# Optimization experiments

Hardware: AMD Instinct MI355X
Metric: run time of the kernel (lower is better)

Reference implementation:

```python
import jax, jax.numpy as jnp
import numpy as np

C = 1280  # layers_dim[1]


def setup_inputs() -> dict:
    key = jax.random.key(0)
    ks = jax.random.split(key, 8)
    E, N, H, W = 8192, 1024, 4, 4
    pose = jax.random.normal(ks[0], (E, 9), dtype=jnp.float32)
    image = jax.random.normal(ks[1], (N, C, H, W), dtype=jnp.float32)
    # edge_encoder params: Linear(9,1280) -> ReLU -> Linear(1280,2560) -> Sigmoid
    W1 = jax.random.normal(ks[2], (9, C), dtype=jnp.float32) * (1.0 / np.sqrt(9))
    b1 = jnp.zeros((C,), dtype=jnp.float32)
    W2 = jax.random.normal(ks[3], (C, 2 * C), dtype=jnp.float32) * (1.0 / np.sqrt(C))
    b2 = jnp.zeros((2 * C,), dtype=jnp.float32)
    src = jax.random.randint(ks[4], (E,), 0, N)
    dst = jax.random.randint(ks[5], (E,), 0, N)
    return {"pose": pose, "image": image, "W1": W1, "b1": b1,
            "W2": W2, "b2": b2, "src": src, "dst": dst}


def reference(pose, image, W1, b1, W2, b2, src, dst):
    # edge encoder: MLP -> sigmoid -> interleaved (gamma, beta) per channel
    h = jax.nn.relu(pose @ W1 + b1)                        # [E, C]
    e = jax.nn.sigmoid(h @ W2 + b2).reshape(-1, C, 2)      # [E, C, 2]
    gamma = e[:, :, 0][:, :, None, None]                   # [E, C, 1, 1]
    beta = e[:, :, 1][:, :, None, None]                    # [E, C, 1, 1]
    # per-edge message: affine transform of source node feature map
    m = gamma * image[src] + beta                          # [E, C, H, W]
    N = image.shape[0]
    s = jax.ops.segment_sum(m, dst, num_segments=N)        # [N, C, H, W]
    cnt = jax.ops.segment_sum(jnp.ones((m.shape[0],), m.dtype), dst,
                              num_segments=N)              # [N]
    cnt4 = cnt[:, None, None, None]
    # mean over mailbox; nodes with no incoming edges stay zero (DGL default)
    return jnp.where(cnt4 > 0, s / jnp.maximum(cnt4, 1.0), 0.0)
```

## Files before the change

### kernel.cpp

```cpp
#include <hip/hip_runtime.h>

#define C_DIM 1280
#define K_DIM 1280
#define N_DIM 2560
#define HWSZ 16
#define CHW (C_DIM*HWSZ)

#define GBM 256
#define GBN 320
#define GBK 64
#define GNT (K_DIM / GBK)

#define EPB 32
#define NBC 2048

typedef __bf16 bf16;
typedef __attribute__((ext_vector_type(8))) __bf16 bf16x8;
typedef __attribute__((ext_vector_type(4))) __bf16 bf16x4;
typedef __attribute__((ext_vector_type(8))) unsigned short u16x8;
typedef __attribute__((ext_vector_type(4))) float f32x4;

template<int V> struct IC { static constexpr int v = V; };

__device__ __forceinline__ void gload_lds16(const void* g, void* l) {
  __builtin_amdgcn_global_load_lds(
      (const __attribute__((address_space(1))) void*)g,
      (__attribute__((address_space(3))) void*)l, 16, 0, 0);
}

#define SB __builtin_amdgcn_sched_barrier(0)

__global__ __launch_bounds__(256) void prep(
    const float* __restrict__ pose, const float* __restrict__ W1,
    const float* __restrict__ b1, bf16* __restrict__ h,
    const float* __restrict__ W2, bf16* __restrict__ W2t,
    const float* __restrict__ img32, bf16* __restrict__ imgb,
    const int* __restrict__ dst, const int* __restrict__ src,
    int* __restrict__ offsets, int2* __restrict__ pairs, int E, int N)
{
  const int b = blockIdx.x;
  const int t = threadIdx.x;
  const int NBP = (E / EPB) * 5;
  const int NBT = (N_DIM / 32) * (K_DIM / 32);

  if (b == 0) {
    __shared__ int cnt[1024];
    __shared__ int cur[1024];
    __shared__ int wsum[4];
    #pragma unroll
    for (int i = 0; i < 4; ++i) cnt[t + 256 * i] = 0;
    __syncthreads();
    const int4* dst4 = (const int4*)dst;
    const int4* src4 = (const int4*)src;
    const int E4 = E >> 2;
    for (int e4 = t; e4 < E4; e4 += 256) {
      const int4 d = dst4[e4];
      atomicAdd(&cnt[d.x], 1); atomicAdd(&cnt[d.y], 1);
      atomicAdd(&cnt[d.z], 1); atomicAdd(&cnt[d.w], 1);
    }
    __syncthreads();
    const int s0 = cnt[4*t], s1 = cnt[4*t+1], s2 = cnt[4*t+2], s3 = cnt[4*t+3];
    const int tot = s0 + s1 + s2 + s3;
    const int lane = t & 63, w = t >> 6;
    int x = tot;
    #pragma unroll
    for (int off = 1; off < 64; off <<= 1) {
      int y = __shfl_up(x, off);
      if (lane >= off) x += y;
    }
    if (lane == 63) wsum[w] = x;
    __syncthreads();
    int woff = 0;
    for (int i = 0; i < w; ++i) woff += wsum[i];
    const int excl = x + woff - tot;
    const int o0 = excl, o1 = o0 + s0, o2 = o1 + s1, o3 = o2 + s2;
    offsets[4*t] = o0; offsets[4*t+1] = o1; offsets[4*t+2] = o2; offsets[4*t+3] = o3;
    cur[4*t] = o0; cur[4*t+1] = o1; cur[4*t+2] = o2; cur[4*t+3] = o3;
    if (t == 0) offsets[N] = E;
    __syncthreads();
    for (int e4 = t; e4 < E4; e4 += 256) {
      const int4 d = dst4[e4];
      const int4 s = src4[e4];
      const int e = e4 * 4;
      int p;
      p = atomicAdd(&cur[d.x], 1); pairs[p] = make_int2(e,     s.x);
      p = atomicAdd(&cur[d.y], 1); pairs[p] = make_int2(e + 1, s.y);
      p = atomicAdd(&cur[d.z], 1); pairs[p] = make_int2(e + 2, s.z);
      p = atomicAdd(&cur[d.w], 1); pairs[p] = make_int2(e + 3, s.w);
    }
    return;
  }

  const int pb = b - 1;
  if (pb < NBP) {
    const int eg = pb / 5;
    const int cc = pb % 5;
    const int c  = cc * 256 + t;
    const int e0 = eg * EPB;
    float w[9];
    #pragma unroll
    for (int k = 0; k < 9; ++k) w[k] = W1[k * C_DIM + c];
    const float bias = b1[c];
    #pragma unroll 4
    for (int i = 0; i < EPB; ++i) {
      const float* p = pose + (size_t)(e0 + i) * 9;
      float s = bias;
      #pragma unroll
      for (int k = 0; k < 9; ++k) s += p[k] * w[k];
      s = s > 0.f ? s : 0.f;
      h[(size_t)(e0 + i) * C_DIM + c] = (bf16)s;
    }
    return;
  }

  if (pb < NBP + NBT) {
    const int tb = pb - NBP;
    __shared__ float tile[32][33];
    const int n0 = (tb % (N_DIM / 32)) * 32;
    const int k0 = (tb / (N_DIM / 32)) * 32;
    const int r  = t >> 3;
    const int c4 = (t & 7) * 4;
    const f32x4 v = *(const f32x4*)(W2 + (size_t)(k0 + r) * N_DIM + n0 + c4);
    tile[r][c4] = v[0]; tile[r][c4+1] = v[1]; tile[r][c4+2] = v[2]; tile[r][c4+3] = v[3];
    __syncthreads();
    bf16x4 o;
    o[0] = (bf16)tile[c4+0][r];
    o[1] = (bf16)tile[c4+1][r];
    o[2] = (bf16)tile[c4+2][r];
    o[3] = (bf16)tile[c4+3][r];
    *(bf16x4*)(W2t + (size_t)(n0 + r) * K_DIM + k0 + c4) = o;
    return;
  }

  const int cb = pb - NBP - NBT;
  f32x4 va[5], vb[5];
  #pragma unroll
  for (int j = 0; j < 5; ++j) {
    const size_t i = ((size_t)(cb + j * NBC) * 256 + t) * 8;
    va[j] = *(const f32x4*)(img32 + i);
    vb[j] = *(const f32x4*)(img32 + i + 4);
  }
  #pragma unroll
  for (int j = 0; j < 5; ++j) {
    const size_t i = ((size_t)(cb + j * NBC) * 256 + t) * 8;
    bf16x8 o;
    o[0]=(bf16)va[j][0]; o[1]=(bf16)va[j][1]; o[2]=(bf16)va[j][2]; o[3]=(bf16)va[j][3];
    o[4]=(bf16)vb[j][0]; o[5]=(bf16)vb[j][1]; o[6]=(bf16)vb[j][2]; o[7]=(bf16)vb[j][3];
    *(bf16x8*)(imgb + i) = o;
  }
}

__global__ __launch_bounds__(512, 2) void gemm_sigmoid(
    const bf16* __restrict__ A, const bf16* __restrict__ Bt,
    const float* __restrict__ b2, bf16* __restrict__ Eo)
{
  __shared__ __align__(16) char Asm[2][GBM * GBK * 2];
  __shared__ __align__(16) char Bsm[2][GBN * GBK * 2];

  const int tid  = threadIdx.x;
  const int lane = tid & 63;
  const int wid  = tid >> 6;
  const int wr   = wid >> 2;
  const int wc   = wid & 3;
  const int fr   = lane & 15;
  const int q    = lane >> 4;
  const int sw   = fr & 7;
  const int g0   = ((q ^ sw) << 4);
  const int g1   = (((4 + q) ^ sw) << 4);

  const int swzb = (blockIdx.x & 7) * 32 + (blockIdx.x >> 3);
  const int mb   = swzb >> 3;
  const int nb   = swzb & 7;
  const long bm  = (long)mb * GBM;
  const long bn  = (long)nb * GBN;

  const bf16* Agl = A  + bm * K_DIM;
  const bf16* Bgl = Bt + bn * K_DIM;

  f32x4 acc[8][5];
  #pragma unroll
  for (int m = 0; m < 8; m++)
    #pragma unroll
    for (int n = 0; n < 5; n++) acc[m][n] = f32x4{0.f, 0.f, 0.f, 0.f};

  auto STAGE_A = [&](int tt, int buf, int u) {
    const int G = u * 512 + tid;
    const int row = G >> 3, g = G & 7;
    const int kg = (g ^ (row & 7)) << 3;
    gload_lds16(Agl + (size_t)row * K_DIM + tt * GBK + kg, Asm[buf] + (size_t)G * 16);
  };
  auto STAGE_B = [&](int tt, int buf, int u) {
    const int G = u * 512 + tid;
    const int row = G >> 3, g = G & 7;
    const int kg = (g ^ (row & 7)) << 3;
    gload_lds16(Bgl + (size_t)row * K_DIM + tt * GBK + kg, Bsm[buf] + (size_t)G * 16);
  };

  STAGE_B(0,0,0); STAGE_B(0,0,1); STAGE_A(0,0,0);
  STAGE_B(0,0,2); STAGE_B(0,0,3); STAGE_A(0,0,2); STAGE_B(0,0,4);
  STAGE_A(0,0,1); STAGE_A(0,0,3);
  asm volatile("s_waitcnt vmcnt(2)" ::: "memory");
  SB;
  __builtin_amdgcn_s_barrier();
  SB;

  auto tile_body = [&](auto PFc, int t) {
    constexpr bool PF = (bool)decltype(PFc)::v;
    const int cur = t & 1;
    const int nxt = cur ^ 1;
    const int tn  = t + 1;
    const char* Ab = Asm[cur];
    const char* Bb = Bsm[cur];

    bf16x8 bfr[5][2];

    auto do_phase = [&](auto Pc) {
      constexpr int p = decltype(Pc)::v;
      if constexpr (p == 0) {
        #pragma unroll
        for (int n = 0; n < 5; ++n) {
          const int rb = (wc * 80 + n * 16 + fr) << 7;
          bfr[n][0] = *(const bf16x8*)(Bb + rb + g0);
          bfr[n][1] = *(const bf16x8*)(Bb + rb + g1);
        }
      }
      bf16x8 a[2][2];
      #pragma unroll
      for (int mm = 0; mm < 2; ++mm) {
        const int ra = (wr * 128 + (2 * p + mm) * 16 + fr) << 7;
        a[mm][0] = *(const bf16x8*)(Ab + ra + g0);
        a[mm][1] = *(const bf16x8*)(Ab + ra + g1);
      }
      if constexpr (PF) {
        if constexpr (p == 0) { STAGE_B(tn,nxt,0); STAGE_B(tn,nxt,1); STAGE_A(tn,nxt,0); }
        if constexpr (p == 1) { STAGE_B(tn,nxt,2); STAGE_B(tn,nxt,3); STAGE_A(tn,nxt,2); STAGE_B(tn,nxt,4); }
        if constexpr (p == 2) { STAGE_A(tn,nxt,1); }
        if constexpr (p == 3) { STAGE_A(tn,nxt,3); }
      }
      SB;
      __builtin_amdgcn_s_barrier();
      asm volatile("s_waitcnt lgkmcnt(0)" ::: "memory");
      SB;
      __builtin_amdgcn_s_setprio(1);
      #pragma unroll
      for (int mm = 0; mm < 2; ++mm)
        #pragma unroll
        for (int n = 0; n < 5; ++n) {
          acc[2*p+mm][n] = __builtin_amdgcn_mfma_f32_16x16x32_bf16(a[mm][0], bfr[n][0], acc[2*p+mm][n], 0, 0, 0);
          acc[2*p+mm][n] = __builtin_amdgcn_mfma_f32_16x16x32_bf16(a[mm][1], bfr[n][1], acc[2*p+mm][n], 0, 0, 0);
        }
      __builtin_amdgcn_s_setprio(0);
      SB;
      if constexpr (p == 1) {
        if constexpr (PF) asm volatile("s_waitcnt vmcnt(7)" ::: "memory");
        else              asm volatile("s_waitcnt vmcnt(0)" ::: "memory");
        SB;
      }
      if constexpr (p == 3 && PF) {
        asm volatile("s_waitcnt vmcnt(2)" ::: "memory");
        SB;
      }
      __builtin_amdgcn_s_barrier();
      SB;
    };

    do_phase(IC<0>{});
    do_phase(IC<1>{});
    do_phase(IC<2>{});
    do_phase(IC<3>{});
  };

  for (int t = 0; t < GNT - 1; ++t) tile_body(IC<1>{}, t);
  tile_body(IC<0>{}, GNT - 1);

  #pragma unroll
  for (int m = 0; m < 8; ++m) {
    const long rowb = bm + wr * 128 + m * 16 + q * 4;
    #pragma unroll
    for (int n = 0; n < 5; ++n) {
      const long col = bn + wc * 80 + n * 16 + fr;
      const float bias = b2[col];
      #pragma unroll
      for (int r = 0; r < 4; ++r) {
        float v = acc[m][n][r] + bias;
        Eo[(rowb + r) * N_DIM + col] = (bf16)(1.f / (1.f + __expf(-v)));
      }
    }
  }
}

__global__ __launch_bounds__(256) void scatter_mean(
    const ushort* __restrict__ Eo,
    const ushort* __restrict__ imgb16,
    const int2* __restrict__ pairs,
    const int* __restrict__ offsets,
    float* __restrict__ out)
{
  const int n = blockIdx.x;
  const int c0 = blockIdx.y * 128;
  const int t = threadIdx.x;
  const int q = t & 1;
  const int cl = t >> 1;
  const int ca = c0 + cl;
  const int ioff = ca * HWSZ + q * 8;

  const int beg = offsets[n], end = offsets[n + 1];
  f32x4 aA0{0.f,0.f,0.f,0.f}, aA1{0.f,0.f,0.f,0.f};
  f32x4 aB0{0.f,0.f,0.f,0.f}, aB1{0.f,0.f,0.f,0.f};

  int2 p0{0,0}, p1{0,0};
  if (beg < end) p0 = pairs[beg];
  if (beg + 1 < end) p1 = pairs[beg + 1];

  auto edge = [&](int2 cp, f32x4& x0, f32x4& x1) {
    const u16x8 iv = *(const u16x8*)(imgb16 + (size_t)cp.y * CHW + ioff);
    const uint u = *(const uint*)(Eo + (size_t)cp.x * N_DIM + 2 * ca);
    const float g  = __uint_as_float(u << 16);
    const float be = __uint_as_float(u & 0xffff0000u);
    f32x4 i0, i1;
    i0[0] = __uint_as_float((uint)iv[0] << 16);
    i0[1] = __uint_as_float((uint)iv[1] << 16);
    i0[2] = __uint_as_float((uint)iv[2] << 16);
    i0[3] = __uint_as_float((uint)iv[3] << 16);
    i1[0] = __uint_as_float((uint)iv[4] << 16);
    i1[1] = __uint_as_float((uint)iv[5] << 16);
    i1[2] = __uint_as_float((uint)iv[6] << 16);
    i1[3] = __uint_as_float((uint)iv[7] << 16);
    x0 += g * i0 + be;
    x1 += g * i1 + be;
  };

  int ei = beg;
  for (; ei + 1 < end; ei += 2) {
    const int2 c0p = p0, c1p = p1;
    if (ei + 2 < end) p0 = pairs[ei + 2];
    if (ei + 3 < end) p1 = pairs[ei + 3];
    edge(c0p, aA0, aA1);
    edge(c1p, aB0, aB1);
  }
  if (ei < end) edge(p0, aA0, aA1);

  const int cnt = end - beg;
  const float inv = cnt > 0 ? 1.f / (float)cnt : 0.f;
  const f32x4 r0 = (aA0 + aB0) * inv;
  const f32x4 r1 = (aA1 + aB1) * inv;
  float* ob = out + (size_t)n * CHW + ioff;
  __builtin_nontemporal_store(r0, (f32x4*)ob);
  __builtin_nontemporal_store(r1, (f32x4*)(ob + 4));
}

extern "C" void kernel_launch(void* const* d_in, const int* in_sizes, int n_in,
                              void* d_out, int out_size, void* d_ws, size_t ws_size,
                              hipStream_t stream) {
  const float* pose  = (const float*)d_in[0];
  const float* image = (const float*)d_in[1];
  const float* W1    = (const float*)d_in[2];
  const float* b1    = (const float*)d_in[3];
  const float* W2    = (const float*)d_in[4];
  const float* b2    = (const float*)d_in[5];
  const int*   src   = (const int*)d_in[6];
  const int*   dst   = (const int*)d_in[7];
  const int E = in_sizes[6];
  const int N = in_sizes[1] / CHW;
  float* out = (float*)d_out;

  char* ws = (char*)d_ws;
  size_t off = 0;
  auto alloc = [&](size_t bytes) {
    void* p = ws + off;
    off = (off + bytes + 255) & ~(size_t)255;
    return p;
  };
  bf16* h     = (bf16*)alloc((size_t)E * C_DIM * sizeof(bf16));
  bf16* W2t   = (bf16*)alloc((size_t)N_DIM * K_DIM * sizeof(bf16));
  bf16* Eout  = (bf16*)alloc((size_t)E * N_DIM * sizeof(bf16));
  bf16* imgb  = (bf16*)alloc((size_t)N * CHW * sizeof(bf16));
  int* offs   = (int*)alloc((size_t)(N + 1) * sizeof(int));
  int2* pairs = (int2*)alloc((size_t)E * sizeof(int2));

  const int nb_prep = 1 + (E / EPB) * 5 + (N_DIM / 32) * (K_DIM / 32) + NBC;
  prep<<<nb_prep, 256, 0, stream>>>(pose, W1, b1, h, W2, W2t, image, imgb,
                                    dst, src, offs, pairs, E, N);

  gemm_sigmoid<<<(E / GBM) * (N_DIM / GBN), 512, 0, stream>>>(h, W2t, b2, Eout);

  scatter_mean<<<dim3(N, 10), 256, 0, stream>>>(
      (const ushort*)Eout, (const ushort*)imgb, pairs, offs, out);
}
```

Baseline: 142.8 us.

## Split CSR build across two prep kernels with global-atomic histogram

Splits the single prep kernel into two launches. The dst histogram is now computed by 8 extra blocks in the first kernel using global atomics on a memset buffer. The second kernel does the scan and pair scatter in one block, using global atomics on a cursor array, alongside the image bf16 conversion. This is meant to shorten the serial single-block critical path that previously did the histogram, scan and scatter alone. In exchange it adds a memset, an extra kernel launch, and slower global atomics in the scatter.

```diff
diff --git a/kernel.cpp b/kernel.cpp
--- a/kernel.cpp
+++ b/kernel.cpp
@@ -30,71 +30,20 @@
 
 #define SB __builtin_amdgcn_sched_barrier(0)
 
-__global__ __launch_bounds__(256) void prep(
+__global__ __launch_bounds__(256) void prep1(
     const float* __restrict__ pose, const float* __restrict__ W1,
     const float* __restrict__ b1, bf16* __restrict__ h,
     const float* __restrict__ W2, bf16* __restrict__ W2t,
-    const float* __restrict__ img32, bf16* __restrict__ imgb,
-    const int* __restrict__ dst, const int* __restrict__ src,
-    int* __restrict__ offsets, int2* __restrict__ pairs, int E, int N)
+    const int* __restrict__ dst, int* __restrict__ cnt_g, int E)
 {
   const int b = blockIdx.x;
   const int t = threadIdx.x;
   const int NBP = (E / EPB) * 5;
   const int NBT = (N_DIM / 32) * (K_DIM / 32);
 
-  if (b == 0) {
-    __shared__ int cnt[1024];
-    __shared__ int cur[1024];
-    __shared__ int wsum[4];
-    #pragma unroll
-    for (int i = 0; i < 4; ++i) cnt[t + 256 * i] = 0;
-    __syncthreads();
-    const int4* dst4 = (const int4*)dst;
-    const int4* src4 = (const int4*)src;
-    const int E4 = E >> 2;
-    for (int e4 = t; e4 < E4; e4 += 256) {
-      const int4 d = dst4[e4];
-      atomicAdd(&cnt[d.x], 1); atomicAdd(&cnt[d.y], 1);
-      atomicAdd(&cnt[d.z], 1); atomicAdd(&cnt[d.w], 1);
-    }
-    __syncthreads();
-    const int s0 = cnt[4*t], s1 = cnt[4*t+1], s2 = cnt[4*t+2], s3 = cnt[4*t+3];
-    const int tot = s0 + s1 + s2 + s3;
-    const int lane = t & 63, w = t >> 6;
-    int x = tot;
-    #pragma unroll
-    for (int off = 1; off < 64; off <<= 1) {
-      int y = __shfl_up(x, off);
-      if (lane >= off) x += y;
-    }
-    if (lane == 63) wsum[w] = x;
-    __syncthreads();
-    int woff = 0;
-    for (int i = 0; i < w; ++i) woff += wsum[i];
-    const int excl = x + woff - tot;
-    const int o0 = excl, o1 = o0 + s0, o2 = o1 + s1, o3 = o2 + s2;
-    offsets[4*t] = o0; offsets[4*t+1] = o1; offsets[4*t+2] = o2; offsets[4*t+3] = o3;
-    cur[4*t] = o0; cur[4*t+1] = o1; cur[4*t+2] = o2; cur[4*t+3] = o3;
-    if (t == 0) offsets[N] = E;
-    __syncthreads();
-    for (int e4 = t; e4 < E4; e4 += 256) {
-      const int4 d = dst4[e4];
-      const int4 s = src4[e4];
-      const int e = e4 * 4;
-      int p;
-      p = atomicAdd(&cur[d.x], 1); pairs[p] = make_int2(e,     s.x);
-      p = atomicAdd(&cur[d.y], 1); pairs[p] = make_int2(e + 1, s.y);
-      p = atomicAdd(&cur[d.z], 1); pairs[p] = make_int2(e + 2, s.z);
-      p = atomicAdd(&cur[d.w], 1); pairs[p] = make_int2(e + 3, s.w);
-    }
-    return;
-  }
-
-  const int pb = b - 1;
-  if (pb < NBP) {
-    const int eg = pb / 5;
-    const int cc = pb % 5;
+  if (b < NBP) {
+    const int eg = b / 5;
+    const int cc = b % 5;
     const int c  = cc * 256 + t;
     const int e0 = eg * EPB;
     float w[9];
@@ -113,8 +62,8 @@
     return;
   }
 
-  if (pb < NBP + NBT) {
-    const int tb = pb - NBP;
+  if (b < NBP + NBT) {
+    const int tb = b - NBP;
     __shared__ float tile[32][33];
     const int n0 = (tb % (N_DIM / 32)) * 32;
     const int k0 = (tb / (N_DIM / 32)) * 32;
@@ -132,7 +81,61 @@
     return;
   }
 
-  const int cb = pb - NBP - NBT;
+  const int hb = b - NBP - NBT;
+  const int e4 = hb * 256 + t;
+  const int4 d = ((const int4*)dst)[e4];
+  atomicAdd(&cnt_g[d.x], 1); atomicAdd(&cnt_g[d.y], 1);
+  atomicAdd(&cnt_g[d.z], 1); atomicAdd(&cnt_g[d.w], 1);
+}
+
+__global__ __launch_bounds__(256) void prep2(
+    const float* __restrict__ img32, bf16* __restrict__ imgb,
+    const int* __restrict__ dst, const int* __restrict__ src,
+    const int* __restrict__ cnt_g, int* __restrict__ cur_g,
+    int* __restrict__ offsets, int2* __restrict__ pairs, int E, int N)
+{
+  const int b = blockIdx.x;
+  const int t = threadIdx.x;
+
+  if (b == 0) {
+    __shared__ int wsum[4];
+    const int4 sv = ((const int4*)cnt_g)[t];
+    const int s0 = sv.x, s1 = sv.y, s2 = sv.z, s3 = sv.w;
+    const int tot = s0 + s1 + s2 + s3;
+    const int lane = t & 63, w = t >> 6;
+    int x = tot;
+    #pragma unroll
+    for (int off = 1; off < 64; off <<= 1) {
+      int y = __shfl_up(x, off);
+      if (lane >= off) x += y;
+    }
+    if (lane == 63) wsum[w] = x;
+    __syncthreads();
+    int woff = 0;
+    for (int i = 0; i < w; ++i) woff += wsum[i];
+    const int excl = x + woff - tot;
+    const int o0 = excl, o1 = o0 + s0, o2 = o1 + s1, o3 = o2 + s2;
+    offsets[4*t] = o0; offsets[4*t+1] = o1; offsets[4*t+2] = o2; offsets[4*t+3] = o3;
+    cur_g[4*t] = o0; cur_g[4*t+1] = o1; cur_g[4*t+2] = o2; cur_g[4*t+3] = o3;
+    if (t == 0) offsets[N] = E;
+    __syncthreads();
+    const int4* dst4 = (const int4*)dst;
+    const int4* src4 = (const int4*)src;
+    const int E4 = E >> 2;
+    for (int e4 = t; e4 < E4; e4 += 256) {
+      const int4 d = dst4[e4];
+      const int4 s = src4[e4];
+      const int e = e4 * 4;
+      int p;
+      p = atomicAdd(&cur_g[d.x], 1); pairs[p] = make_int2(e,     s.x);
+      p = atomicAdd(&cur_g[d.y], 1); pairs[p] = make_int2(e + 1, s.y);
+      p = atomicAdd(&cur_g[d.z], 1); pairs[p] = make_int2(e + 2, s.z);
+      p = atomicAdd(&cur_g[d.w], 1); pairs[p] = make_int2(e + 3, s.w);
+    }
+    return;
+  }
+
+  const int cb = b - 1;
   f32x4 va[5], vb[5];
   #pragma unroll
   for (int j = 0; j < 5; ++j) {
@@ -377,10 +380,16 @@
   bf16* imgb  = (bf16*)alloc((size_t)N * CHW * sizeof(bf16));
   int* offs   = (int*)alloc((size_t)(N + 1) * sizeof(int));
   int2* pairs = (int2*)alloc((size_t)E * sizeof(int2));
-
-  const int nb_prep = 1 + (E / EPB) * 5 + (N_DIM / 32) * (K_DIM / 32) + NBC;
-  prep<<<nb_prep, 256, 0, stream>>>(pose, W1, b1, h, W2, W2t, image, imgb,
-                                    dst, src, offs, pairs, E, N);
+  int* cnt_g  = (int*)alloc((size_t)N * sizeof(int));
+  int* cur_g  = (int*)alloc((size_t)N * sizeof(int));
+
+  hipMemsetAsync(cnt_g, 0, (size_t)N * sizeof(int), stream);
+
+  const int nb1 = (E / EPB) * 5 + (N_DIM / 32) * (K_DIM / 32) + 8;
+  prep1<<<nb1, 256, 0, stream>>>(pose, W1, b1, h, W2, W2t, dst, cnt_g, E);
+
+  prep2<<<1 + NBC, 256, 0, stream>>>(image, imgb, dst, src, cnt_g, cur_g,
+                                     offs, pairs, E, N);
 
   gemm_sigmoid<<<(E / GBM) * (N_DIM / GBN), 512, 0, stream>>>(h, W2t, b2, Eout);
 
```

Measured after the change: 161.5 us. 13.1% more time.
